# Kernel tuning notes

Hardware: AMD Instinct MI355X
Metric: run time of the kernel (lower is better)

Reference implementation:

```python
import jax, jax.numpy as jnp
import numpy as np

N_NODES = 100000
SAMPLES = 16


def setup_inputs() -> dict:
    key = jax.random.key(0)
    ks = jax.random.split(key, 9)
    x = jax.random.normal(ks[0], (N_NODES, 128), dtype=jnp.float32)
    neigh_idx = jax.random.randint(ks[1], (N_NODES, SAMPLES), 0, N_NODES)
    batch = jax.random.randint(ks[2], (8192,), 0, N_NODES)
    W1 = jax.random.normal(ks[3], (256, 128), dtype=jnp.float32) * 0.05
    b1 = jax.random.normal(ks[4], (128,), dtype=jnp.float32) * 0.05
    W2 = jax.random.normal(ks[5], (256, 128), dtype=jnp.float32) * 0.05
    b2 = jax.random.normal(ks[6], (128,), dtype=jnp.float32) * 0.05
    Wout = jax.random.normal(ks[7], (128, 64), dtype=jnp.float32) * 0.05
    bout = jax.random.normal(ks[8], (64,), dtype=jnp.float32) * 0.05
    return {"x": x, "neigh_idx": neigh_idx, "batch": batch,
            "W1": W1, "b1": b1, "W2": W2, "b2": b2,
            "Wout": Wout, "bout": bout}


def _sage_layer(h, neigh_idx, W, b):
    # h: [N, d]; gather sampled neighbors -> [N, S, d]; max-aggregate; concat-linear
    neigh = h[neigh_idx]                     # irregular gather, memory-bound core
    agg = jnp.max(neigh, axis=1)             # MaxAggregation over samples
    feats = jnp.concatenate([h, agg], axis=-1)  # [N, 2d]
    return feats @ W + b


def reference(x, neigh_idx, batch, W1, b1, W2, b2, Wout, bout):
    # layer 1: relu(Linear(concat(x, max_neigh(x))))
    h1 = jax.nn.relu(_sage_layer(x, neigh_idx, W1, b1))
    # layer 2 (== n_layers): Linear output (no relu) fed straight into proj_out
    h2 = _sage_layer(h1, neigh_idx, W2, b2)
    out = h2 @ Wout + bout                   # proj_out (Dropout is eval identity)
    return out[batch]
```

## Files before the change

### kernel.cpp

```cpp
#include <hip/hip_runtime.h>
#include <cmath>
#include <cstdint>

#define N_NODES 100000
#define SAMPLES 16
#define DIM 128
#define NBATCH 8192

#define FSTR 264
#define H2STR 132

typedef _Float16 half8 __attribute__((ext_vector_type(8)));
typedef float floatx4 __attribute__((ext_vector_type(4)));

__device__ __forceinline__ half8 h8max(half8 a, half8 b) {
    half8 r;
#pragma unroll
    for (int i = 0; i < 8; ++i) r[i] = (a[i] > b[i]) ? a[i] : b[i];
    return r;
}

__global__ void zero_flags(int* __restrict__ flags) {
    int i = blockIdx.x * blockDim.x + threadIdx.x;
    if (i < N_NODES) flags[i] = 0;
}

__global__ void mark_flags(const int* __restrict__ batch,
                           const int* __restrict__ nidx,
                           int* __restrict__ flags) {
    int j = blockIdx.x * blockDim.x + threadIdx.x;
    if (j >= NBATCH) return;
    int b = batch[j];
    flags[b] = 1;
    const int* row = nidx + (size_t)b * SAMPLES;
#pragma unroll
    for (int s = 0; s < SAMPLES; ++s) flags[row[s]] = 1;
}

__global__ __launch_bounds__(256) void cvt_x(const float* __restrict__ x,
                                             _Float16* __restrict__ xh) {
    const int tid = blockIdx.x * blockDim.x + threadIdx.x;
    const size_t base = (size_t)tid * 8;
    if (base >= (size_t)N_NODES * DIM) return;
    const float4* xp = (const float4*)(x + base);
    const float4 a = xp[0], b = xp[1];
    half8 v;
    v[0] = (_Float16)a.x; v[1] = (_Float16)a.y;
    v[2] = (_Float16)a.z; v[3] = (_Float16)a.w;
    v[4] = (_Float16)b.x; v[5] = (_Float16)b.y;
    v[6] = (_Float16)b.z; v[7] = (_Float16)b.w;
    *(half8*)(xh + base) = v;
}

__global__ __launch_bounds__(256) void swizzle_w(const float* __restrict__ W1,
                                                 const float* __restrict__ W2,
                                                 _Float16* __restrict__ W1sw,
                                                 _Float16* __restrict__ W2sw) {
    const int tid = blockIdx.x * blockDim.x + threadIdx.x;
    const int which = tid >> 12;
    const int r = tid & 4095;
    const int kb = r >> 9, nb = (r >> 6) & 7, lane = r & 63;
    const int q = lane >> 4, c = lane & 15;
    const float* W = which ? W2 : W1;
    _Float16* O = which ? W2sw : W1sw;
    const int k0 = kb * 32 + q * 8;
    const int n = nb * 16 + c;
    half8 v;
#pragma unroll
    for (int j = 0; j < 8; ++j) v[j] = (_Float16)W[(size_t)(k0 + j) * DIM + n];
    *(half8*)(O + (size_t)r * 8) = v;
}

__global__ __launch_bounds__(256) void layer1_kernel(
    const _Float16* __restrict__ xh,
    const int* __restrict__ nidx,
    const _Float16* __restrict__ W1sw,
    const float* __restrict__ b1,
    const int* __restrict__ flags,
    _Float16* __restrict__ h1h) {
    const int wave = threadIdx.x >> 6;
    const int lane = threadIdx.x & 63;
    const int q = lane >> 4;
    const int c = lane & 15;
    const int w0 = blockIdx.x * 64 + wave * 16;

    __shared__ __align__(16) _Float16 feats[4][16 * FSTR];
    _Float16* fw = feats[wave];

#pragma unroll
    for (int ng = 0; ng < 4; ++ng) {
        const int m = ng * 4 + q;
        const int i = w0 + m;
        const bool valid = (i < N_NODES) && flags[i];
        if (valid) {
            const half8 s = *(const half8*)(xh + (size_t)i * DIM + c * 8);
            *(half8*)(fw + m * FSTR + c * 8) = s;
            half8 mx;
#pragma unroll
            for (int e = 0; e < 8; ++e) mx[e] = (_Float16)(-60000.f);
            const int* row = nidx + (size_t)i * SAMPLES;
#pragma unroll
            for (int s2 = 0; s2 < SAMPLES; ++s2) {
                const int nb = row[s2];
                const half8 v = *(const half8*)(xh + (size_t)nb * DIM + c * 8);
                mx = h8max(mx, v);
            }
            *(half8*)(fw + m * FSTR + DIM + c * 8) = mx;
        }
    }
    __syncthreads();

    floatx4 acc[8];
#pragma unroll
    for (int nb = 0; nb < 8; ++nb) acc[nb] = (floatx4){0.f, 0.f, 0.f, 0.f};

#pragma unroll
    for (int kb = 0; kb < 8; ++kb) {
        const half8 a = *(const half8*)(fw + c * FSTR + kb * 32 + q * 8);
#pragma unroll
        for (int nb = 0; nb < 8; ++nb) {
            const half8 b = *(const half8*)(W1sw + (size_t)((kb * 8 + nb) * 64 + lane) * 8);
            acc[nb] = __builtin_amdgcn_mfma_f32_16x16x32_f16(a, b, acc[nb], 0, 0, 0);
        }
    }

    int fl[4];
#pragma unroll
    for (int r = 0; r < 4; ++r) {
        const int i = w0 + q * 4 + r;
        fl[r] = (i < N_NODES) && flags[i];
    }
#pragma unroll
    for (int nb = 0; nb < 8; ++nb) {
        const int n = nb * 16 + c;
        const float bias = b1[n];
#pragma unroll
        for (int r = 0; r < 4; ++r) {
            if (!fl[r]) continue;
            const int i = w0 + q * 4 + r;
            const float v = fmaxf(acc[nb][r] + bias, 0.f);
            h1h[(size_t)i * DIM + n] = (_Float16)v;
        }
    }
}

__global__ __launch_bounds__(64) void layer2_kernel(
    const _Float16* __restrict__ h1h,
    const int* __restrict__ nidx,
    const int* __restrict__ batch,
    const _Float16* __restrict__ W2sw,
    const float* __restrict__ b2,
    const float* __restrict__ Wout,
    const float* __restrict__ bout,
    float* __restrict__ out) {
    const int lane = threadIdx.x;
    const int q = lane >> 4, c = lane & 15;
    const int w0 = blockIdx.x * 16;

    __shared__ __align__(16) _Float16 feats[16 * FSTR];
    __shared__ __align__(16) float h2s[16 * H2STR];

#pragma unroll
    for (int ng = 0; ng < 4; ++ng) {
        const int m = ng * 4 + q;
        const int node = batch[w0 + m];
        const half8 s = *(const half8*)(h1h + (size_t)node * DIM + c * 8);
        *(half8*)(feats + m * FSTR + c * 8) = s;
        half8 mx;
#pragma unroll
        for (int e = 0; e < 8; ++e) mx[e] = (_Float16)(-60000.f);
        const int* row = nidx + (size_t)node * SAMPLES;
#pragma unroll
        for (int s2 = 0; s2 < SAMPLES; ++s2) {
            const int nb = row[s2];
            const half8 v = *(const half8*)(h1h + (size_t)nb * DIM + c * 8);
            mx = h8max(mx, v);
        }
        *(half8*)(feats + m * FSTR + DIM + c * 8) = mx;
    }
    __syncthreads();

    floatx4 acc[8];
#pragma unroll
    for (int nb = 0; nb < 8; ++nb) acc[nb] = (floatx4){0.f, 0.f, 0.f, 0.f};

#pragma unroll
    for (int kb = 0; kb < 8; ++kb) {
        const half8 a = *(const half8*)(feats + c * FSTR + kb * 32 + q * 8);
#pragma unroll
        for (int nb = 0; nb < 8; ++nb) {
            const half8 b = *(const half8*)(W2sw + (size_t)((kb * 8 + nb) * 64 + lane) * 8);
            acc[nb] = __builtin_amdgcn_mfma_f32_16x16x32_f16(a, b, acc[nb], 0, 0, 0);
        }
    }

#pragma unroll
    for (int nb = 0; nb < 8; ++nb) {
        const float bias = b2[nb * 16 + c];
#pragma unroll
        for (int r = 0; r < 4; ++r)
            h2s[(q * 4 + r) * H2STR + nb * 16 + c] = acc[nb][r] + bias;
    }
    __syncthreads();

    float accs[16];
    const float bo = bout[lane];
#pragma unroll
    for (int m = 0; m < 16; ++m) accs[m] = bo;
    for (int k4 = 0; k4 < DIM; k4 += 4) {
        float wv[4];
#pragma unroll
        for (int j = 0; j < 4; ++j) wv[j] = Wout[(size_t)(k4 + j) * 64 + lane];
#pragma unroll
        for (int m = 0; m < 16; ++m) {
            const float4 f = *(const float4*)&h2s[m * H2STR + k4];
            accs[m] += f.x * wv[0] + f.y * wv[1] + f.z * wv[2] + f.w * wv[3];
        }
    }
#pragma unroll
    for (int m = 0; m < 16; ++m)
        out[(size_t)(w0 + m) * 64 + lane] = accs[m];
}

extern "C" void kernel_launch(void* const* d_in, const int* in_sizes, int n_in,
                              void* d_out, int out_size, void* d_ws, size_t ws_size,
                              hipStream_t stream) {
    const float* x    = (const float*)d_in[0];
    const int* nidx   = (const int*)d_in[1];
    const int* batch  = (const int*)d_in[2];
    const float* W1   = (const float*)d_in[3];
    const float* b1   = (const float*)d_in[4];
    const float* W2   = (const float*)d_in[5];
    const float* b2   = (const float*)d_in[6];
    const float* Wout = (const float*)d_in[7];
    const float* bout = (const float*)d_in[8];
    float* out        = (float*)d_out;

    int* flags      = (int*)d_ws;
    _Float16* W1sw  = (_Float16*)((char*)d_ws + 409600);
    _Float16* W2sw  = (_Float16*)((char*)d_ws + 475136);
    _Float16* xh    = (_Float16*)((char*)d_ws + 540672);
    _Float16* h1h   = (_Float16*)((char*)d_ws + 26140672);

    zero_flags<<<(N_NODES + 255) / 256, 256, 0, stream>>>(flags);
    mark_flags<<<(NBATCH + 255) / 256, 256, 0, stream>>>(batch, nidx, flags);
    cvt_x<<<(N_NODES * DIM / 8 + 255) / 256, 256, 0, stream>>>(x, xh);
    swizzle_w<<<32, 256, 0, stream>>>(W1, W2, W1sw, W2sw);
    layer1_kernel<<<(N_NODES + 63) / 64, 256, 0, stream>>>(xh, nidx, W1sw, b1, flags, h1h);
    layer2_kernel<<<NBATCH / 16, 64, 0, stream>>>(h1h, nidx, batch, W2sw, b2, Wout, bout, out);
}
```

Baseline: 197.9 us.

## Gather MFMA operands into registers directly and fuse setup kernels

Both SAGE layers now have each lane gather its own MFMA A-operand fragments (self row and max over neighbours) straight into registers. This removes the LDS staging buffer and the block barrier between gather and matmul. Neighbour indices are read as int4 vectors, and two neighbour rows are loaded per step to raise memory-level parallelism. The flag zeroing, x conversion and weight swizzle are merged into one setup kernel to cut launch count. In exchange, register pressure goes up, and each lane's loads are strided 16B chunks rather than one contiguous row per quarter-wave.

Measured after the change: 204.4 us. 3.3% more time.

```diff
diff --git a/kernel.cpp b/kernel.cpp
--- a/kernel.cpp
+++ b/kernel.cpp
@@ -7,7 +7,6 @@
 #define DIM 128
 #define NBATCH 8192
 
-#define FSTR 264
 #define H2STR 132
 
 typedef _Float16 half8 __attribute__((ext_vector_type(8)));
@@ -20,14 +19,48 @@
     return r;
 }
 
-__global__ void zero_flags(int* __restrict__ flags) {
-    int i = blockIdx.x * blockDim.x + threadIdx.x;
-    if (i < N_NODES) flags[i] = 0;
-}
-
-__global__ void mark_flags(const int* __restrict__ batch,
-                           const int* __restrict__ nidx,
-                           int* __restrict__ flags) {
+__global__ __launch_bounds__(256) void setup_kernel(
+    const float* __restrict__ x,
+    const float* __restrict__ W1,
+    const float* __restrict__ W2,
+    int* __restrict__ flags,
+    _Float16* __restrict__ xh,
+    _Float16* __restrict__ W1sw,
+    _Float16* __restrict__ W2sw) {
+    const int bid = blockIdx.x;
+    if (bid < 6250) {
+        const size_t base = ((size_t)bid * 256 + threadIdx.x) * 8;
+        const float4* xp = (const float4*)(x + base);
+        const float4 a = xp[0], b = xp[1];
+        half8 v;
+        v[0] = (_Float16)a.x; v[1] = (_Float16)a.y;
+        v[2] = (_Float16)a.z; v[3] = (_Float16)a.w;
+        v[4] = (_Float16)b.x; v[5] = (_Float16)b.y;
+        v[6] = (_Float16)b.z; v[7] = (_Float16)b.w;
+        *(half8*)(xh + base) = v;
+    } else if (bid < 6641) {
+        const int i = (bid - 6250) * 256 + threadIdx.x;
+        if (i < N_NODES) flags[i] = 0;
+    } else {
+        const int tid = (bid - 6641) * 256 + threadIdx.x;
+        const int which = tid >> 12;
+        const int r = tid & 4095;
+        const int kb = r >> 9, nb = (r >> 6) & 7, lane = r & 63;
+        const int q = lane >> 4, c = lane & 15;
+        const float* W = which ? W2 : W1;
+        _Float16* O = which ? W2sw : W1sw;
+        const int k0 = kb * 32 + q * 8;
+        const int n = nb * 16 + c;
+        half8 v;
+#pragma unroll
+        for (int j = 0; j < 8; ++j) v[j] = (_Float16)W[(size_t)(k0 + j) * DIM + n];
+        *(half8*)(O + (size_t)r * 8) = v;
+    }
+}
+
+__global__ __launch_bounds__(256) void mark_flags(const int* __restrict__ batch,
+                                                  const int* __restrict__ nidx,
+                                                  int* __restrict__ flags) {
     int j = blockIdx.x * blockDim.x + threadIdx.x;
     if (j >= NBATCH) return;
     int b = batch[j];
@@ -35,40 +68,6 @@
     const int* row = nidx + (size_t)b * SAMPLES;
 #pragma unroll
     for (int s = 0; s < SAMPLES; ++s) flags[row[s]] = 1;
-}
-
-__global__ __launch_bounds__(256) void cvt_x(const float* __restrict__ x,
-                                             _Float16* __restrict__ xh) {
-    const int tid = blockIdx.x * blockDim.x + threadIdx.x;
-    const size_t base = (size_t)tid * 8;
-    if (base >= (size_t)N_NODES * DIM) return;
-    const float4* xp = (const float4*)(x + base);
-    const float4 a = xp[0], b = xp[1];
-    half8 v;
-    v[0] = (_Float16)a.x; v[1] = (_Float16)a.y;
-    v[2] = (_Float16)a.z; v[3] = (_Float16)a.w;
-    v[4] = (_Float16)b.x; v[5] = (_Float16)b.y;
-    v[6] = (_Float16)b.z; v[7] = (_Float16)b.w;
-    *(half8*)(xh + base) = v;
-}
-
-__global__ __launch_bounds__(256) void swizzle_w(const float* __restrict__ W1,
-                                                 const float* __restrict__ W2,
-                                                 _Float16* __restrict__ W1sw,
-                                                 _Float16* __restrict__ W2sw) {
-    const int tid = blockIdx.x * blockDim.x + threadIdx.x;
-    const int which = tid >> 12;
-    const int r = tid & 4095;
-    const int kb = r >> 9, nb = (r >> 6) & 7, lane = r & 63;
-    const int q = lane >> 4, c = lane & 15;
-    const float* W = which ? W2 : W1;
-    _Float16* O = which ? W2sw : W1sw;
-    const int k0 = kb * 32 + q * 8;
-    const int n = nb * 16 + c;
-    half8 v;
-#pragma unroll
-    for (int j = 0; j < 8; ++j) v[j] = (_Float16)W[(size_t)(k0 + j) * DIM + n];
-    *(half8*)(O + (size_t)r * 8) = v;
 }
 
 __global__ __launch_bounds__(256) void layer1_kernel(
@@ -84,39 +83,45 @@
     const int c = lane & 15;
     const int w0 = blockIdx.x * 64 + wave * 16;
 
-    __shared__ __align__(16) _Float16 feats[4][16 * FSTR];
-    _Float16* fw = feats[wave];
-
-#pragma unroll
-    for (int ng = 0; ng < 4; ++ng) {
-        const int m = ng * 4 + q;
-        const int i = w0 + m;
-        const bool valid = (i < N_NODES) && flags[i];
-        if (valid) {
-            const half8 s = *(const half8*)(xh + (size_t)i * DIM + c * 8);
-            *(half8*)(fw + m * FSTR + c * 8) = s;
-            half8 mx;
-#pragma unroll
-            for (int e = 0; e < 8; ++e) mx[e] = (_Float16)(-60000.f);
-            const int* row = nidx + (size_t)i * SAMPLES;
-#pragma unroll
-            for (int s2 = 0; s2 < SAMPLES; ++s2) {
-                const int nb = row[s2];
-                const half8 v = *(const half8*)(xh + (size_t)nb * DIM + c * 8);
-                mx = h8max(mx, v);
-            }
-            *(half8*)(fw + m * FSTR + DIM + c * 8) = mx;
-        }
-    }
-    __syncthreads();
+    const int i = w0 + c;
+    const bool fi = (i < N_NODES) && flags[i];
+
+    half8 sk[4], mk[4];
+#pragma unroll
+    for (int j = 0; j < 4; ++j) {
+#pragma unroll
+        for (int e = 0; e < 8; ++e) { sk[j][e] = (_Float16)0.f; mk[j][e] = (_Float16)(-60000.f); }
+    }
+
+    if (fi) {
+        const _Float16* rp = xh + (size_t)i * DIM + q * 8;
+#pragma unroll
+        for (int j = 0; j < 4; ++j) sk[j] = *(const half8*)(rp + j * 32);
+
+        const int4* ip = (const int4*)(nidx + (size_t)i * SAMPLES);
+        const int4 i0 = ip[0], i1 = ip[1], i2 = ip[2], i3 = ip[3];
+        const int idx[16] = {i0.x, i0.y, i0.z, i0.w, i1.x, i1.y, i1.z, i1.w,
+                             i2.x, i2.y, i2.z, i2.w, i3.x, i3.y, i3.z, i3.w};
+#pragma unroll
+        for (int s = 0; s < SAMPLES; s += 2) {
+            const _Float16* ra = xh + (size_t)idx[s] * DIM + q * 8;
+            const _Float16* rb = xh + (size_t)idx[s + 1] * DIM + q * 8;
+            half8 va[4], vb[4];
+#pragma unroll
+            for (int j = 0; j < 4; ++j) va[j] = *(const half8*)(ra + j * 32);
+#pragma unroll
+            for (int j = 0; j < 4; ++j) vb[j] = *(const half8*)(rb + j * 32);
+#pragma unroll
+            for (int j = 0; j < 4; ++j) mk[j] = h8max(mk[j], h8max(va[j], vb[j]));
+        }
+    }
 
     floatx4 acc[8];
 #pragma unroll
     for (int nb = 0; nb < 8; ++nb) acc[nb] = (floatx4){0.f, 0.f, 0.f, 0.f};
-
 #pragma unroll
     for (int kb = 0; kb < 8; ++kb) {
-        const half8 a = *(const half8*)(fw + c * FSTR + kb * 32 + q * 8);
+        const half8 a = (kb < 4) ? sk[kb] : mk[kb - 4];
 #pragma unroll
         for (int nb = 0; nb < 8; ++nb) {
             const half8 b = *(const half8*)(W1sw + (size_t)((kb * 8 + nb) * 64 + lane) * 8);
@@ -124,22 +129,15 @@
         }
     }
 
-    int fl[4];
 #pragma unroll
     for (int r = 0; r < 4; ++r) {
-        const int i = w0 + q * 4 + r;
-        fl[r] = (i < N_NODES) && flags[i];
-    }
-#pragma unroll
-    for (int nb = 0; nb < 8; ++nb) {
-        const int n = nb * 16 + c;
-        const float bias = b1[n];
-#pragma unroll
-        for (int r = 0; r < 4; ++r) {
-            if (!fl[r]) continue;
-            const int i = w0 + q * 4 + r;
-            const float v = fmaxf(acc[nb][r] + bias, 0.f);
-            h1h[(size_t)i * DIM + n] = (_Float16)v;
+        const int node = w0 + q * 4 + r;
+        if (node >= N_NODES || !flags[node]) continue;
+#pragma unroll
+        for (int nb = 0; nb < 8; ++nb) {
+            const int n = nb * 16 + c;
+            const float v = fmaxf(acc[nb][r] + b1[n], 0.f);
+            h1h[(size_t)node * DIM + n] = (_Float16)v;
         }
     }
 }
@@ -157,36 +155,42 @@
     const int q = lane >> 4, c = lane & 15;
     const int w0 = blockIdx.x * 16;
 
-    __shared__ __align__(16) _Float16 feats[16 * FSTR];
     __shared__ __align__(16) float h2s[16 * H2STR];
 
-#pragma unroll
-    for (int ng = 0; ng < 4; ++ng) {
-        const int m = ng * 4 + q;
-        const int node = batch[w0 + m];
-        const half8 s = *(const half8*)(h1h + (size_t)node * DIM + c * 8);
-        *(half8*)(feats + m * FSTR + c * 8) = s;
-        half8 mx;
-#pragma unroll
-        for (int e = 0; e < 8; ++e) mx[e] = (_Float16)(-60000.f);
-        const int* row = nidx + (size_t)node * SAMPLES;
-#pragma unroll
-        for (int s2 = 0; s2 < SAMPLES; ++s2) {
-            const int nb = row[s2];
-            const half8 v = *(const half8*)(h1h + (size_t)nb * DIM + c * 8);
-            mx = h8max(mx, v);
-        }
-        *(half8*)(feats + m * FSTR + DIM + c * 8) = mx;
-    }
-    __syncthreads();
+    const int node = batch[w0 + c];
+    half8 sk[4], mk[4];
+    {
+        const _Float16* rp = h1h + (size_t)node * DIM + q * 8;
+#pragma unroll
+        for (int j = 0; j < 4; ++j) sk[j] = *(const half8*)(rp + j * 32);
+#pragma unroll
+        for (int j = 0; j < 4; ++j)
+#pragma unroll
+            for (int e = 0; e < 8; ++e) mk[j][e] = (_Float16)(-60000.f);
+        const int4* ip = (const int4*)(nidx + (size_t)node * SAMPLES);
+        const int4 i0 = ip[0], i1 = ip[1], i2 = ip[2], i3 = ip[3];
+        const int idx[16] = {i0.x, i0.y, i0.z, i0.w, i1.x, i1.y, i1.z, i1.w,
+                             i2.x, i2.y, i2.z, i2.w, i3.x, i3.y, i3.z, i3.w};
+#pragma unroll
+        for (int s = 0; s < SAMPLES; s += 2) {
+            const _Float16* ra = h1h + (size_t)idx[s] * DIM + q * 8;
+            const _Float16* rb = h1h + (size_t)idx[s + 1] * DIM + q * 8;
+            half8 va[4], vb[4];
+#pragma unroll
+            for (int j = 0; j < 4; ++j) va[j] = *(const half8*)(ra + j * 32);
+#pragma unroll
+            for (int j = 0; j < 4; ++j) vb[j] = *(const half8*)(rb + j * 32);
+#pragma unroll
+            for (int j = 0; j < 4; ++j) mk[j] = h8max(mk[j], h8max(va[j], vb[j]));
+        }
+    }
 
     floatx4 acc[8];
 #pragma unroll
     for (int nb = 0; nb < 8; ++nb) acc[nb] = (floatx4){0.f, 0.f, 0.f, 0.f};
-
 #pragma unroll
     for (int kb = 0; kb < 8; ++kb) {
-        const half8 a = *(const half8*)(feats + c * FSTR + kb * 32 + q * 8);
+        const half8 a = (kb < 4) ? sk[kb] : mk[kb - 4];
 #pragma unroll
         for (int nb = 0; nb < 8; ++nb) {
             const half8 b = *(const half8*)(W2sw + (size_t)((kb * 8 + nb) * 64 + lane) * 8);
@@ -196,12 +200,12 @@
 
 #pragma unroll
     for (int nb = 0; nb < 8; ++nb) {
-        const float bias = b2[nb * 16 + c];
+        const int n = nb * 16 + c;
+        const float bias = b2[n];
 #pragma unroll
         for (int r = 0; r < 4; ++r)
-            h2s[(q * 4 + r) * H2STR + nb * 16 + c] = acc[nb][r] + bias;
-    }
-    __syncthreads();
+            h2s[(q * 4 + r) * H2STR + n] = acc[nb][r] + bias;
+    }
 
     float accs[16];
     const float bo = bout[lane];
@@ -242,10 +246,8 @@
     _Float16* xh    = (_Float16*)((char*)d_ws + 540672);
     _Float16* h1h   = (_Float16*)((char*)d_ws + 26140672);
 
-    zero_flags<<<(N_NODES + 255) / 256, 256, 0, stream>>>(flags);
-    mark_flags<<<(NBATCH + 255) / 256, 256, 0, stream>>>(batch, nidx, flags);
-    cvt_x<<<(N_NODES * DIM / 8 + 255) / 256, 256, 0, stream>>>(x, xh);
-    swizzle_w<<<32, 256, 0, stream>>>(W1, W2, W1sw, W2sw);
+    setup_kernel<<<6673, 256, 0, stream>>>(x, W1, W2, flags, xh, W1sw, W2sw);
+    mark_flags<<<32, 256, 0, stream>>>(batch, nidx, flags);
     layer1_kernel<<<(N_NODES + 63) / 64, 256, 0, stream>>>(xh, nidx, W1sw, b1, flags, h1h);
     layer2_kernel<<<NBATCH / 16, 64, 0, stream>>>(h1h, nidx, batch, W2sw, b2, Wout, bout, out);
 }
```
